# Kernel tuning notes

Hardware: AMD Instinct MI355X
Metric: run time of the kernel (lower is better)

Reference implementation:

```python
import jax, jax.numpy as jnp
import numpy as np

B = 128        # graphs
NPG = 64       # nodes per graph (num_node)
N = B * NPG    # total nodes = 8192
IN = 16        # in_channels
D = 128        # d_model
OUT = 64       # out_channels
CAT = IN * NPG + NPG * NPG  # 5120
EPS = 1e-5


def _lin_init(k, fi, fo):
    s = 1.0 / np.sqrt(fi)
    kw, kb = jax.random.split(k)
    W = jax.random.uniform(kw, (fi, fo), jnp.float32, -s, s)
    b = jax.random.uniform(kb, (fo,), jnp.float32, -s, s)
    return W, b


def setup_inputs() -> dict:
    key = jax.random.key(0)
    ks = jax.random.split(key, 10)
    x = jax.random.normal(ks[0], (N, IN), jnp.float32)
    # complete graph (all i->j pairs, incl. self loops) per graph, offset per graph
    ii = np.repeat(np.arange(NPG), NPG)
    jj = np.tile(np.arange(NPG), NPG)
    off = (np.arange(B) * NPG)[:, None]
    row = (ii[None, :] + off).reshape(-1)
    col = (jj[None, :] + off).reshape(-1)
    edge_index = jnp.asarray(np.stack([row, col]), jnp.int32)  # [2, E]
    E = edge_index.shape[1]
    edge_weight = jax.random.uniform(ks[1], (E,), jnp.float32)
    batch = jnp.repeat(jnp.arange(B, dtype=jnp.int32), NPG)
    W1, b1 = _lin_init(ks[2], IN, D)
    W2, b2 = _lin_init(ks[3], D, D)
    Wm0, bm0 = _lin_init(ks[4], D + CAT, D)
    Wm1, bm1 = _lin_init(ks[5], D, D)
    Wm2, bm2 = _lin_init(ks[6], D, D)
    Wout, bout = _lin_init(ks[7], D, OUT)
    ones = jnp.ones((D,), jnp.float32)
    zeros = jnp.zeros((D,), jnp.float32)
    return dict(x=x, edge_index=edge_index, edge_weight=edge_weight, batch=batch,
                W1=W1, b1=b1, W2=W2, b2=b2,
                Wm0=Wm0, bm0=bm0, g0=ones, be0=zeros,
                Wm1=Wm1, bm1=bm1, g1=ones, be1=zeros,
                Wm2=Wm2, bm2=bm2, g2=ones, be2=zeros,
                Wout=Wout, bout=bout)


def _gcn_conv(h_in, row, col, ew, W, b):
    # PyG GCNConv: linear first, then D^-1/2 (A) D^-1/2 aggregation (self loops already present)
    h = h_in @ W                                             # [N, F]
    deg = jax.ops.segment_sum(ew, col, num_segments=N)       # in-degree by edge weight
    dinv = jnp.where(deg > 0, jax.lax.rsqrt(deg), 0.0)
    norm = dinv[row] * ew * dinv[col]                        # [E]
    out = jax.ops.segment_sum(norm[:, None] * h[row], col, num_segments=N)
    return out + b


def _bn(h, g, b):
    # BatchNorm1d, training-mode math (biased variance), eps=1e-5
    m = jnp.mean(h, axis=0)
    v = jnp.var(h, axis=0)
    return g * (h - m) * jax.lax.rsqrt(v + EPS) + b


def reference(x, edge_index, edge_weight, batch,
              W1, b1, W2, b2,
              Wm0, bm0, g0, be0,
              Wm1, bm1, g1, be1,
              Wm2, bm2, g2, be2,
              Wout, bout):
    row, col = edge_index[0], edge_index[1]
    h = _gcn_conv(x, row, col, edge_weight, W1, b1)
    h = jax.nn.relu(h)
    h = _gcn_conv(h, row, col, edge_weight, W2, b2)
    # global_mean_pool
    sums = jax.ops.segment_sum(h, batch, num_segments=B)
    cnt = jax.ops.segment_sum(jnp.ones((N,), h.dtype), batch, num_segments=B)
    pooled = sums / cnt[:, None]
    pooled = jax.nn.relu(pooled)
    feat = jnp.concatenate([pooled, x.reshape(B, -1), edge_weight.reshape(B, -1)], axis=1)
    feat = jax.nn.relu(feat)
    h = _bn(jax.nn.relu(feat @ Wm0 + bm0), g0, be0)
    h = _bn(jax.nn.relu(h @ Wm1 + bm1), g1, be1)
    h = _bn(jax.nn.relu(h @ Wm2 + bm2), g2, be2)
    return h @ Wout + bout
```

## Files before the change

### kernel.cpp

```cpp
#include <hip/hip_runtime.h>

#define NG 128
#define NPG 64
#define IN 16
#define DM 128
#define NOUT 64
#define EPG 4096
#define NGEMM 160
#define BN_EPS 1e-5f

__global__ __launch_bounds__(256) void k_front(
    const float* __restrict__ x, const float* __restrict__ ew,
    const float* __restrict__ W1, const float* __restrict__ b1,
    const float* __restrict__ Wm0,
    float* __restrict__ z, float* __restrict__ part, float* __restrict__ stats)
{
    __shared__ __align__(16) float u[12544];
    const int b = blockIdx.x, t = threadIdx.x;

    if (b < 256) {
        float* ew_s   = u;
        float* x_s    = u + 4096;
        float* W1h_s  = u + 5120;
        float* P_s    = u + 6144;
        float* b1h_s  = u + 10240;
        float* dinv_s = u + 10304;
        float* t_s    = u + 10368;
        const int g = b >> 1, half = b & 1, fh0 = half * 64;
        if (b == 0) {
            for (int i = t; i < 768; i += 256) stats[i] = 0.f;
        }
        {
            const float4* ew4 = (const float4*)(ew + g * EPG);
            float4* ews4 = (float4*)ew_s;
            #pragma unroll
            for (int i = 0; i < 4; i++) ews4[t + 256 * i] = ew4[t + 256 * i];
            ((float4*)x_s)[t] = ((const float4*)(x + g * NPG * IN))[t];
        }
        for (int i = t; i < IN * 64; i += 256)
            W1h_s[i] = W1[(i >> 6) * DM + fh0 + (i & 63)];
        if (t < 64) b1h_s[t] = b1[fh0 + t];
        __syncthreads();

        if (t < NPG) {
            float s = 0.f;
            #pragma unroll 8
            for (int i = 0; i < NPG; i++) s += ew_s[i * NPG + t];
            dinv_s[t] = (s > 0.f) ? rsqrtf(s) : 0.f;
        }
        __syncthreads();

        {
            const int j = t & 63, q = t >> 6;
            const float dj = dinv_s[j];
            for (int i = q * 16; i < q * 16 + 16; i++) {
                float vv = ew_s[i * NPG + j] * dj;
                #pragma unroll
                for (int off = 32; off > 0; off >>= 1) vv += __shfl_down(vv, off, 64);
                if (j == 0) t_s[i] = dinv_s[i] * vv * (1.f / 64.f);
            }
        }

        {
            const int f = t & 63, ih = t >> 6;
            for (int i = ih * 16; i < ih * 16 + 16; i++) {
                float acc = 0.f;
                #pragma unroll
                for (int k = 0; k < IN; k++) acc += x_s[i * IN + k] * W1h_s[k * 64 + f];
                P_s[i * 64 + f] = acc;
            }
        }
        __syncthreads();

        for (int i = t; i < EPG; i += 256) ew_s[i] *= dinv_s[i >> 6];
        __syncthreads();

        {
            const int j = t & 63, q = t >> 6, fb = q * 16;
            float acc[16];
            #pragma unroll
            for (int uu = 0; uu < 16; uu++) acc[uu] = 0.f;
            for (int i = 0; i < NPG; i++) {
                const float w = ew_s[i * NPG + j];
                const float4* p4 = (const float4*)(P_s + i * 64 + fb);
                #pragma unroll
                for (int u4 = 0; u4 < 4; u4++) {
                    float4 p = p4[u4];
                    acc[4 * u4 + 0] += w * p.x;
                    acc[4 * u4 + 1] += w * p.y;
                    acc[4 * u4 + 2] += w * p.z;
                    acc[4 * u4 + 3] += w * p.w;
                }
            }
            const float dj = dinv_s[j], tj = t_s[j];
            #pragma unroll
            for (int uu = 0; uu < 16; uu++) {
                float h = fmaxf(dj * acc[uu] + b1h_s[fb + uu], 0.f);
                float zv = tj * h;
                #pragma unroll
                for (int off = 32; off > 0; off >>= 1) zv += __shfl_down(zv, off, 64);
                if (j == 0) z[g * DM + fh0 + fb + uu] = zv;
            }
        }
    } else {
        const int c = b - 256;
        const int kc = c >> 1, fh = c & 1;
        float* a_s = u;
        float* b_s = u + 8448;

        const float* src; int stride, off;
        if (kc < 16) { src = x;  stride = 1024; off = kc * 64; }
        else         { src = ew; stride = 4096; off = (kc - 16) * 64; }
        const int K0 = 128 + kc * 64;

        #pragma unroll 4
        for (int it = 0; it < 32; it++) {
            int idx = it * 256 + t;
            int gg = idx >> 6, k = idx & 63;
            a_s[k * 132 + gg] = fmaxf(src[gg * stride + off + k], 0.f);
        }
        #pragma unroll 4
        for (int it = 0; it < 16; it++) {
            int idx = it * 256 + t;
            int k = idx >> 6, fl = idx & 63;
            b_s[k * 64 + fl] = Wm0[(K0 + k) * 128 + fh * 64 + fl];
        }
        __syncthreads();

        const int gthr = t & 31, fthr = t >> 5;
        const int g0 = gthr * 4, f0 = fthr * 8;
        float acc[4][8];
        #pragma unroll
        for (int i = 0; i < 4; i++)
            #pragma unroll
            for (int jx = 0; jx < 8; jx++) acc[i][jx] = 0.f;

        #pragma unroll 4
        for (int k = 0; k < 64; k++) {
            const float4 a4  = *(const float4*)(a_s + k * 132 + g0);
            const float4 c0v = *(const float4*)(b_s + k * 64 + f0);
            const float4 c1v = *(const float4*)(b_s + k * 64 + f0 + 4);
            const float av[4] = {a4.x, a4.y, a4.z, a4.w};
            const float bv[8] = {c0v.x, c0v.y, c0v.z, c0v.w, c1v.x, c1v.y, c1v.z, c1v.w};
            #pragma unroll
            for (int i = 0; i < 4; i++)
                #pragma unroll
                for (int jx = 0; jx < 8; jx++) acc[i][jx] += av[i] * bv[jx];
        }

        float* pp = part + c * 8192;
        #pragma unroll
        for (int i = 0; i < 4; i++) {
            float4* o = (float4*)(pp + (g0 + i) * 64 + f0);
            o[0] = make_float4(acc[i][0], acc[i][1], acc[i][2], acc[i][3]);
            o[1] = make_float4(acc[i][4], acc[i][5], acc[i][6], acc[i][7]);
        }
    }
}

__global__ __launch_bounds__(256) void k_reduce_bn0(
    const float* __restrict__ part, const float* __restrict__ zbuf,
    const float* __restrict__ W2, const float* __restrict__ b2,
    const float* __restrict__ Wm0, const float* __restrict__ bm0,
    float* __restrict__ v0, float* __restrict__ stats0)
{
    __shared__ __align__(16) float W2_s[16384];
    __shared__ __align__(16) float z_s[512];
    __shared__ float Wm0s[2048];
    __shared__ float pooled_s[4 * 130];
    __shared__ float pps[64];
    __shared__ float r1[256];
    __shared__ float sv[64], sv2[64];

    const int bx = blockIdx.x, t = threadIdx.x;
    const int fgrp = bx & 7, gt = bx >> 3;
    const int fsub = t & 15, gl = (t >> 4) & 3, ch = t >> 6;
    const int f = fgrp * 16 + fsub, g = gt * 4 + gl;
    const int fh = f >> 6, fl = f & 63;

    const float* p = part + (size_t)(2 * (ch * 20) + fh) * 8192 + g * 64 + fl;
    float v = 0.f;
    #pragma unroll 5
    for (int cc = 0; cc < 20; cc++) v += p[(size_t)cc * 2 * 8192];

    {
        const float4* w24 = (const float4*)W2;
        float4* w2s4 = (float4*)W2_s;
        #pragma unroll
        for (int i = 0; i < 16; i++) w2s4[t + 256 * i] = w24[t + 256 * i];
        if (t < 128) ((float4*)z_s)[t] = ((const float4*)(zbuf + gt * 512))[t];
        for (int idx = t; idx < 2048; idx += 256) {
            int k = idx >> 4, fs = idx & 15;
            Wm0s[idx] = Wm0[k * DM + fgrp * 16 + fs];
        }
    }
    r1[t] = v;
    __syncthreads();

    {
        const int gp = t >> 6, k0 = t & 63;
        float a0 = 0.f, a1 = 0.f;
        #pragma unroll 4
        for (int m = 0; m < DM; m++) {
            const float zm = z_s[gp * DM + m];
            a0 += zm * W2_s[m * DM + k0];
            a1 += zm * W2_s[m * DM + k0 + 64];
        }
        pooled_s[gp * 130 + k0]      = fmaxf(a0 + b2[k0], 0.f);
        pooled_s[gp * 130 + k0 + 64] = fmaxf(a1 + b2[k0 + 64], 0.f);
    }
    __syncthreads();

    if (t < 64) {
        const int gl2 = t >> 4, fs = t & 15;
        float a = 0.f;
        #pragma unroll 8
        for (int k = 0; k < DM; k++) a += pooled_s[gl2 * 130 + k] * Wm0s[k * 16 + fs];
        pps[t] = a;
    }
    __syncthreads();

    if (ch == 0) {
        v = r1[t] + r1[t + 64] + r1[t + 128] + r1[t + 192]
          + bm0[f] + pps[t];
        v = fmaxf(v, 0.f);
        v0[g * DM + f] = v;
        sv[t] = v; sv2[t] = v * v;
    }
    __syncthreads();
    if (t < 16) {
        float s1 = sv[t] + sv[t + 16] + sv[t + 32] + sv[t + 48];
        float s2 = sv2[t] + sv2[t + 16] + sv2[t + 32] + sv2[t + 48];
        atomicAdd(&stats0[(fgrp * 16 + t) * 2], s1);
        atomicAdd(&stats0[(fgrp * 16 + t) * 2 + 1], s2);
    }
}

__global__ __launch_bounds__(256) void k_mlp(
    const float* __restrict__ vin, const float* __restrict__ statsin,
    const float* __restrict__ gbn, const float* __restrict__ bbn,
    const float* __restrict__ W, const float* __restrict__ bias,
    float* __restrict__ vout, float* __restrict__ statsout)
{
    __shared__ float h_s[128 * 129];
    __shared__ float wcol[128];
    __shared__ float scale_s[128], shift_s[128];
    __shared__ float pc[128];
    __shared__ float rr[4];
    const int f = blockIdx.x, t = threadIdx.x;
    if (t < 128) {
        float s1 = statsin[t * 2], s2 = statsin[t * 2 + 1];
        float m = s1 * (1.f / 128.f);
        float var = s2 * (1.f / 128.f) - m * m;
        float sc = gbn[t] * rsqrtf(var + BN_EPS);
        scale_s[t] = sc;
        shift_s[t] = bbn[t] - m * sc;
        wcol[t] = W[t * 128 + f];
    }
    __syncthreads();
    #pragma unroll 4
    for (int it = 0; it < 16; it++) {
        int idx = it * 256 + t;
        int g = idx >> 5, k4 = (idx & 31) * 4;
        float4 vv = ((const float4*)vin)[idx];
        float* hp = h_s + g * 129 + k4;
        hp[0] = vv.x * scale_s[k4 + 0] + shift_s[k4 + 0];
        hp[1] = vv.y * scale_s[k4 + 1] + shift_s[k4 + 1];
        hp[2] = vv.z * scale_s[k4 + 2] + shift_s[k4 + 2];
        hp[3] = vv.w * scale_s[k4 + 3] + shift_s[k4 + 3];
    }
    __syncthreads();
    const int g = t & 127, kh = t >> 7;
    float acc = 0.f;
    #pragma unroll 8
    for (int k = kh * 64; k < kh * 64 + 64; k++) acc += h_s[g * 129 + k] * wcol[k];
    if (kh) pc[g] = acc;
    __syncthreads();
    if (t < 128) {
        float v = fmaxf(acc + pc[t] + bias[f], 0.f);
        vout[t * 128 + f] = v;
        float s1 = v, s2 = v * v;
        #pragma unroll
        for (int off = 32; off > 0; off >>= 1) {
            s1 += __shfl_down(s1, off, 64);
            s2 += __shfl_down(s2, off, 64);
        }
        if ((t & 63) == 0) { rr[(t >> 6) * 2] = s1; rr[(t >> 6) * 2 + 1] = s2; }
    }
    __syncthreads();
    if (t == 0) {
        statsout[f * 2]     = rr[0] + rr[2];
        statsout[f * 2 + 1] = rr[1] + rr[3];
    }
}

__global__ __launch_bounds__(128) void k_out(
    const float* __restrict__ vin, const float* __restrict__ statsin,
    const float* __restrict__ gbn, const float* __restrict__ bbn,
    const float* __restrict__ Wo, const float* __restrict__ bo,
    float* __restrict__ out)
{
    __shared__ __align__(16) float Wo_s[128 * 64];
    __shared__ float vrow[2][128];
    __shared__ float scale_s[128], shift_s[128];
    const int b = blockIdx.x, t = threadIdx.x, g0 = b * 2;
    {
        float s1 = statsin[t * 2], s2 = statsin[t * 2 + 1];
        float m = s1 * (1.f / 128.f);
        float var = s2 * (1.f / 128.f) - m * m;
        float sc = gbn[t] * rsqrtf(var + BN_EPS);
        scale_s[t] = sc;
        shift_s[t] = bbn[t] - m * sc;
    }
    __syncthreads();
    {
        const float4* wo4 = (const float4*)Wo;
        float4* wos4 = (float4*)Wo_s;
        #pragma unroll
        for (int it = 0; it < 16; it++) wos4[it * 128 + t] = wo4[it * 128 + t];
    }
    if (t < 64) {
        int g2 = t >> 5, k4 = (t & 31) * 4;
        float4 vv = ((const float4*)(vin + g0 * 128))[t];
        vrow[g2][k4 + 0] = vv.x * scale_s[k4 + 0] + shift_s[k4 + 0];
        vrow[g2][k4 + 1] = vv.y * scale_s[k4 + 1] + shift_s[k4 + 1];
        vrow[g2][k4 + 2] = vv.z * scale_s[k4 + 2] + shift_s[k4 + 2];
        vrow[g2][k4 + 3] = vv.w * scale_s[k4 + 3] + shift_s[k4 + 3];
    }
    __syncthreads();
    const int g2 = t >> 6, o = t & 63;
    float acc = bo[o];
    #pragma unroll 8
    for (int k = 0; k < 128; k++) acc += vrow[g2][k] * Wo_s[k * 64 + o];
    out[(g0 + g2) * NOUT + o] = acc;
}

extern "C" void kernel_launch(void* const* d_in, const int* in_sizes, int n_in,
                              void* d_out, int out_size, void* d_ws, size_t ws_size,
                              hipStream_t stream)
{
    const float* x   = (const float*)d_in[0];
    const float* ew  = (const float*)d_in[2];
    const float* W1  = (const float*)d_in[4];
    const float* b1  = (const float*)d_in[5];
    const float* W2  = (const float*)d_in[6];
    const float* b2  = (const float*)d_in[7];
    const float* Wm0 = (const float*)d_in[8];
    const float* bm0 = (const float*)d_in[9];
    const float* g0  = (const float*)d_in[10];
    const float* be0 = (const float*)d_in[11];
    const float* Wm1 = (const float*)d_in[12];
    const float* bm1 = (const float*)d_in[13];
    const float* g1  = (const float*)d_in[14];
    const float* be1 = (const float*)d_in[15];
    const float* Wm2 = (const float*)d_in[16];
    const float* bm2 = (const float*)d_in[17];
    const float* g2  = (const float*)d_in[18];
    const float* be2 = (const float*)d_in[19];
    const float* Wo  = (const float*)d_in[20];
    const float* bo  = (const float*)d_in[21];

    float* ws     = (float*)d_ws;
    float* zbuf   = ws;
    float* part   = zbuf + 16384;
    float* v0     = part + NGEMM * 8192;
    float* v1     = v0 + 16384;
    float* v2     = v1 + 16384;
    float* stats  = v2 + 16384;

    k_front<<<256 + NGEMM, 256, 0, stream>>>(x, ew, W1, b1, Wm0, zbuf, part, stats);
    k_reduce_bn0<<<256, 256, 0, stream>>>(part, zbuf, W2, b2, Wm0, bm0, v0, stats);
    k_mlp<<<128, 256, 0, stream>>>(v0, stats,       g0, be0, Wm1, bm1, v1, stats + 256);
    k_mlp<<<128, 256, 0, stream>>>(v1, stats + 256, g1, be1, Wm2, bm2, v2, stats + 512);
    k_out<<<NOUT, 128, 0, stream>>>(v2, stats + 512, g2, be2, Wo, bo, (float*)d_out);
}
```

Baseline: 140.4 us.

## Fuse all stages into one persistent kernel with grid-wide atomic barriers

Replaces five kernel launches with a single 256-block kernel that runs the GCN front, the split-K Wm0 GEMM, the BN0 reduction, two MLP stages and the output layer in sequence, separated by software grid barriers built on atomics. The Wm0 GEMM is re-split into 256 chunks of 40 K-values so every block does both the front work and a GEMM slice. The MLP stages now split graphs across two blocks per feature and accumulate BN statistics with atomics. A memset zeroes the stats and barrier counters beforehand. This removes launch gaps and kernel boundaries, at the cost of relying on all 256 blocks being co-resident and of serialising the front and GEMM work inside each block.

```diff
diff --git a/kernel.cpp b/kernel.cpp
--- a/kernel.cpp
+++ b/kernel.cpp
@@ -6,19 +6,104 @@
 #define DM 128
 #define NOUT 64
 #define EPG 4096
-#define NGEMM 160
 #define BN_EPS 1e-5f
-
-__global__ __launch_bounds__(256) void k_front(
+#define NBLK 256
+
+__device__ __forceinline__ void gbar(unsigned* bar, int idx) {
+    __syncthreads();
+    if (threadIdx.x == 0) {
+        __threadfence();
+        __hip_atomic_fetch_add(&bar[idx], 1u, __ATOMIC_ACQ_REL, __HIP_MEMORY_SCOPE_AGENT);
+        while (__hip_atomic_load(&bar[idx], __ATOMIC_ACQUIRE, __HIP_MEMORY_SCOPE_AGENT) < (unsigned)NBLK) {
+            __builtin_amdgcn_s_sleep(2);
+        }
+        __threadfence();
+    }
+    __syncthreads();
+}
+
+__device__ __forceinline__ void mlp_stage(
+    float* u, const float* __restrict__ vin, const float* __restrict__ statsin,
+    const float* __restrict__ gbn, const float* __restrict__ bbn,
+    const float* __restrict__ W, const float* __restrict__ bias,
+    float* __restrict__ vout, float* __restrict__ statsout)
+{
+    float* scale_s = u;
+    float* shift_s = u + 128;
+    float* wcol    = u + 256;
+    float* pc      = u + 384;
+    float* h_s     = u + 640;
+    const int b = blockIdx.x, t = threadIdx.x;
+    const int f = b & 127, gh = b >> 7;
+    if (t < 128) {
+        float s1 = statsin[t * 2], s2 = statsin[t * 2 + 1];
+        float m = s1 * (1.f / 128.f);
+        float var = s2 * (1.f / 128.f) - m * m;
+        float sc = gbn[t] * rsqrtf(var + BN_EPS);
+        scale_s[t] = sc;
+        shift_s[t] = bbn[t] - m * sc;
+        wcol[t] = W[t * 128 + f];
+    }
+    __syncthreads();
+    const int g0r = gh * 64;
+    const float4* vin4 = (const float4*)(vin + g0r * 128);
+    #pragma unroll
+    for (int it = 0; it < 8; ++it) {
+        int idx = it * 256 + t;
+        int gl = idx >> 5, k4 = (idx & 31) * 4;
+        float4 vv = vin4[idx];
+        float* hp = h_s + gl * 129 + k4;
+        hp[0] = vv.x * scale_s[k4 + 0] + shift_s[k4 + 0];
+        hp[1] = vv.y * scale_s[k4 + 1] + shift_s[k4 + 1];
+        hp[2] = vv.z * scale_s[k4 + 2] + shift_s[k4 + 2];
+        hp[3] = vv.w * scale_s[k4 + 3] + shift_s[k4 + 3];
+    }
+    __syncthreads();
+    {
+        const int gl = t & 63, kh = t >> 6;
+        float acc = 0.f;
+        #pragma unroll 8
+        for (int k = kh * 32; k < kh * 32 + 32; ++k) acc += h_s[gl * 129 + k] * wcol[k];
+        pc[gl * 4 + kh] = acc;
+    }
+    __syncthreads();
+    if (t < 64) {
+        float v = fmaxf(pc[t * 4] + pc[t * 4 + 1] + pc[t * 4 + 2] + pc[t * 4 + 3]
+                        + bias[f], 0.f);
+        vout[(size_t)(g0r + t) * 128 + f] = v;
+        float s1 = v, s2 = v * v;
+        #pragma unroll
+        for (int off = 32; off > 0; off >>= 1) {
+            s1 += __shfl_down(s1, off, 64);
+            s2 += __shfl_down(s2, off, 64);
+        }
+        if (t == 0) {
+            atomicAdd(&statsout[f * 2], s1);
+            atomicAdd(&statsout[f * 2 + 1], s2);
+        }
+    }
+}
+
+__global__ __launch_bounds__(256, 2) void k_all(
     const float* __restrict__ x, const float* __restrict__ ew,
     const float* __restrict__ W1, const float* __restrict__ b1,
-    const float* __restrict__ Wm0,
-    float* __restrict__ z, float* __restrict__ part, float* __restrict__ stats)
+    const float* __restrict__ W2, const float* __restrict__ b2,
+    const float* __restrict__ Wm0, const float* __restrict__ bm0,
+    const float* __restrict__ g0bn, const float* __restrict__ be0,
+    const float* __restrict__ Wm1, const float* __restrict__ bm1,
+    const float* __restrict__ g1bn, const float* __restrict__ be1,
+    const float* __restrict__ Wm2, const float* __restrict__ bm2,
+    const float* __restrict__ g2bn, const float* __restrict__ be2,
+    const float* __restrict__ Wo, const float* __restrict__ bo,
+    float* __restrict__ z, float* __restrict__ part,
+    float* __restrict__ v0, float* __restrict__ v1, float* __restrict__ v2,
+    float* __restrict__ stats, unsigned* __restrict__ bar,
+    float* __restrict__ out)
 {
-    __shared__ __align__(16) float u[12544];
+    __shared__ __align__(16) float u[19968];
     const int b = blockIdx.x, t = threadIdx.x;
 
-    if (b < 256) {
+    {
         float* ew_s   = u;
         float* x_s    = u + 4096;
         float* W1h_s  = u + 5120;
@@ -27,9 +112,6 @@
         float* dinv_s = u + 10304;
         float* t_s    = u + 10368;
         const int g = b >> 1, half = b & 1, fh0 = half * 64;
-        if (b == 0) {
-            for (int i = t; i < 768; i += 256) stats[i] = 0.f;
-        }
         {
             const float4* ew4 = (const float4*)(ew + g * EPG);
             float4* ews4 = (float4*)ew_s;
@@ -60,7 +142,6 @@
                 if (j == 0) t_s[i] = dinv_s[i] * vv * (1.f / 64.f);
             }
         }
-
         {
             const int f = t & 63, ih = t >> 6;
             for (int i = ih * 16; i < ih * 16 + 16; i++) {
@@ -102,28 +183,27 @@
                 if (j == 0) z[g * DM + fh0 + fb + uu] = zv;
             }
         }
-    } else {
-        const int c = b - 256;
-        const int kc = c >> 1, fh = c & 1;
+        __syncthreads();
+    }
+
+    {
+        const int kc = b >> 1, fh = b & 1;
+        const int K0 = kc * 40;
         float* a_s = u;
-        float* b_s = u + 8448;
-
-        const float* src; int stride, off;
-        if (kc < 16) { src = x;  stride = 1024; off = kc * 64; }
-        else         { src = ew; stride = 4096; off = (kc - 16) * 64; }
-        const int K0 = 128 + kc * 64;
+        float* b_s = u + 5280;
 
         #pragma unroll 4
-        for (int it = 0; it < 32; it++) {
+        for (int it = 0; it < 20; ++it) {
             int idx = it * 256 + t;
-            int gg = idx >> 6, k = idx & 63;
-            a_s[k * 132 + gg] = fmaxf(src[gg * stride + off + k], 0.f);
+            int k = idx >> 7, gg = idx & 127;
+            int K = K0 + k;
+            float val = (K < 1024) ? x[gg * 1024 + K] : ew[gg * 4096 + (K - 1024)];
+            a_s[k * 132 + gg] = fmaxf(val, 0.f);
         }
         #pragma unroll 4
-        for (int it = 0; it < 16; it++) {
-            int idx = it * 256 + t;
+        for (int idx = t; idx < 2560; idx += 256) {
             int k = idx >> 6, fl = idx & 63;
-            b_s[k * 64 + fl] = Wm0[(K0 + k) * 128 + fh * 64 + fl];
+            b_s[k * 64 + fl] = Wm0[(128 + K0 + k) * 128 + fh * 64 + fl];
         }
         __syncthreads();
 
@@ -136,7 +216,7 @@
             for (int jx = 0; jx < 8; jx++) acc[i][jx] = 0.f;
 
         #pragma unroll 4
-        for (int k = 0; k < 64; k++) {
+        for (int k = 0; k < 40; k++) {
             const float4 a4  = *(const float4*)(a_s + k * 132 + g0);
             const float4 c0v = *(const float4*)(b_s + k * 64 + f0);
             const float4 c1v = *(const float4*)(b_s + k * 64 + f0 + 4);
@@ -147,8 +227,7 @@
                 #pragma unroll
                 for (int jx = 0; jx < 8; jx++) acc[i][jx] += av[i] * bv[jx];
         }
-
-        float* pp = part + c * 8192;
+        float* pp = part + (size_t)b * 8192;
         #pragma unroll
         for (int i = 0; i < 4; i++) {
             float4* o = (float4*)(pp + (g0 + i) * 64 + f0);
@@ -156,183 +235,121 @@
             o[1] = make_float4(acc[i][4], acc[i][5], acc[i][6], acc[i][7]);
         }
     }
-}
-
-__global__ __launch_bounds__(256) void k_reduce_bn0(
-    const float* __restrict__ part, const float* __restrict__ zbuf,
-    const float* __restrict__ W2, const float* __restrict__ b2,
-    const float* __restrict__ Wm0, const float* __restrict__ bm0,
-    float* __restrict__ v0, float* __restrict__ stats0)
-{
-    __shared__ __align__(16) float W2_s[16384];
-    __shared__ __align__(16) float z_s[512];
-    __shared__ float Wm0s[2048];
-    __shared__ float pooled_s[4 * 130];
-    __shared__ float pps[64];
-    __shared__ float r1[256];
-    __shared__ float sv[64], sv2[64];
-
-    const int bx = blockIdx.x, t = threadIdx.x;
-    const int fgrp = bx & 7, gt = bx >> 3;
-    const int fsub = t & 15, gl = (t >> 4) & 3, ch = t >> 6;
-    const int f = fgrp * 16 + fsub, g = gt * 4 + gl;
-    const int fh = f >> 6, fl = f & 63;
-
-    const float* p = part + (size_t)(2 * (ch * 20) + fh) * 8192 + g * 64 + fl;
-    float v = 0.f;
-    #pragma unroll 5
-    for (int cc = 0; cc < 20; cc++) v += p[(size_t)cc * 2 * 8192];
+    gbar(bar, 0);
 
     {
-        const float4* w24 = (const float4*)W2;
-        float4* w2s4 = (float4*)W2_s;
-        #pragma unroll
-        for (int i = 0; i < 16; i++) w2s4[t + 256 * i] = w24[t + 256 * i];
-        if (t < 128) ((float4*)z_s)[t] = ((const float4*)(zbuf + gt * 512))[t];
-        for (int idx = t; idx < 2048; idx += 256) {
-            int k = idx >> 4, fs = idx & 15;
-            Wm0s[idx] = Wm0[k * DM + fgrp * 16 + fs];
-        }
-    }
-    r1[t] = v;
-    __syncthreads();
-
-    {
-        const int gp = t >> 6, k0 = t & 63;
-        float a0 = 0.f, a1 = 0.f;
-        #pragma unroll 4
-        for (int m = 0; m < DM; m++) {
-            const float zm = z_s[gp * DM + m];
-            a0 += zm * W2_s[m * DM + k0];
-            a1 += zm * W2_s[m * DM + k0 + 64];
-        }
-        pooled_s[gp * 130 + k0]      = fmaxf(a0 + b2[k0], 0.f);
-        pooled_s[gp * 130 + k0 + 64] = fmaxf(a1 + b2[k0 + 64], 0.f);
-    }
-    __syncthreads();
-
-    if (t < 64) {
-        const int gl2 = t >> 4, fs = t & 15;
-        float a = 0.f;
+        float* W2_s     = u;
+        float* z_s      = u + 16384;
+        float* Wm0s     = u + 16896;
+        float* pooled_s = u + 18944;
+        float* pps      = u + 19464;
+        float* r1       = u + 19528;
+        float* sv       = u + 19784;
+        float* sv2      = u + 19848;
+        const int fgrp = b & 7, gt = b >> 3;
+        const int fsub = t & 15, gl = (t >> 4) & 3, ch = t >> 6;
+        const int f = fgrp * 16 + fsub, g = gt * 4 + gl;
+        const int fh = f >> 6, fl = f & 63;
+
+        const float* p = part + (size_t)(2 * (ch * 32) + fh) * 8192 + g * 64 + fl;
+        float v = 0.f;
         #pragma unroll 8
-        for (int k = 0; k < DM; k++) a += pooled_s[gl2 * 130 + k] * Wm0s[k * 16 + fs];
-        pps[t] = a;
-    }
-    __syncthreads();
-
-    if (ch == 0) {
-        v = r1[t] + r1[t + 64] + r1[t + 128] + r1[t + 192]
-          + bm0[f] + pps[t];
-        v = fmaxf(v, 0.f);
-        v0[g * DM + f] = v;
-        sv[t] = v; sv2[t] = v * v;
-    }
-    __syncthreads();
-    if (t < 16) {
-        float s1 = sv[t] + sv[t + 16] + sv[t + 32] + sv[t + 48];
-        float s2 = sv2[t] + sv2[t + 16] + sv2[t + 32] + sv2[t + 48];
-        atomicAdd(&stats0[(fgrp * 16 + t) * 2], s1);
-        atomicAdd(&stats0[(fgrp * 16 + t) * 2 + 1], s2);
-    }
-}
-
-__global__ __launch_bounds__(256) void k_mlp(
-    const float* __restrict__ vin, const float* __restrict__ statsin,
-    const float* __restrict__ gbn, const float* __restrict__ bbn,
-    const float* __restrict__ W, const float* __restrict__ bias,
-    float* __restrict__ vout, float* __restrict__ statsout)
-{
-    __shared__ float h_s[128 * 129];
-    __shared__ float wcol[128];
-    __shared__ float scale_s[128], shift_s[128];
-    __shared__ float pc[128];
-    __shared__ float rr[4];
-    const int f = blockIdx.x, t = threadIdx.x;
-    if (t < 128) {
-        float s1 = statsin[t * 2], s2 = statsin[t * 2 + 1];
-        float m = s1 * (1.f / 128.f);
-        float var = s2 * (1.f / 128.f) - m * m;
-        float sc = gbn[t] * rsqrtf(var + BN_EPS);
-        scale_s[t] = sc;
-        shift_s[t] = bbn[t] - m * sc;
-        wcol[t] = W[t * 128 + f];
-    }
-    __syncthreads();
-    #pragma unroll 4
-    for (int it = 0; it < 16; it++) {
-        int idx = it * 256 + t;
-        int g = idx >> 5, k4 = (idx & 31) * 4;
-        float4 vv = ((const float4*)vin)[idx];
-        float* hp = h_s + g * 129 + k4;
-        hp[0] = vv.x * scale_s[k4 + 0] + shift_s[k4 + 0];
-        hp[1] = vv.y * scale_s[k4 + 1] + shift_s[k4 + 1];
-        hp[2] = vv.z * scale_s[k4 + 2] + shift_s[k4 + 2];
-        hp[3] = vv.w * scale_s[k4 + 3] + shift_s[k4 + 3];
-    }
-    __syncthreads();
-    const int g = t & 127, kh = t >> 7;
-    float acc = 0.f;
-    #pragma unroll 8
-    for (int k = kh * 64; k < kh * 64 + 64; k++) acc += h_s[g * 129 + k] * wcol[k];
-    if (kh) pc[g] = acc;
-    __syncthreads();
-    if (t < 128) {
-        float v = fmaxf(acc + pc[t] + bias[f], 0.f);
-        vout[t * 128 + f] = v;
-        float s1 = v, s2 = v * v;
-        #pragma unroll
-        for (int off = 32; off > 0; off >>= 1) {
-            s1 += __shfl_down(s1, off, 64);
-            s2 += __shfl_down(s2, off, 64);
-        }
-        if ((t & 63) == 0) { rr[(t >> 6) * 2] = s1; rr[(t >> 6) * 2 + 1] = s2; }
-    }
-    __syncthreads();
-    if (t == 0) {
-        statsout[f * 2]     = rr[0] + rr[2];
-        statsout[f * 2 + 1] = rr[1] + rr[3];
-    }
-}
-
-__global__ __launch_bounds__(128) void k_out(
-    const float* __restrict__ vin, const float* __restrict__ statsin,
-    const float* __restrict__ gbn, const float* __restrict__ bbn,
-    const float* __restrict__ Wo, const float* __restrict__ bo,
-    float* __restrict__ out)
-{
-    __shared__ __align__(16) float Wo_s[128 * 64];
-    __shared__ float vrow[2][128];
-    __shared__ float scale_s[128], shift_s[128];
-    const int b = blockIdx.x, t = threadIdx.x, g0 = b * 2;
-    {
-        float s1 = statsin[t * 2], s2 = statsin[t * 2 + 1];
-        float m = s1 * (1.f / 128.f);
-        float var = s2 * (1.f / 128.f) - m * m;
-        float sc = gbn[t] * rsqrtf(var + BN_EPS);
-        scale_s[t] = sc;
-        shift_s[t] = bbn[t] - m * sc;
-    }
-    __syncthreads();
-    {
-        const float4* wo4 = (const float4*)Wo;
-        float4* wos4 = (float4*)Wo_s;
-        #pragma unroll
-        for (int it = 0; it < 16; it++) wos4[it * 128 + t] = wo4[it * 128 + t];
-    }
-    if (t < 64) {
-        int g2 = t >> 5, k4 = (t & 31) * 4;
-        float4 vv = ((const float4*)(vin + g0 * 128))[t];
-        vrow[g2][k4 + 0] = vv.x * scale_s[k4 + 0] + shift_s[k4 + 0];
-        vrow[g2][k4 + 1] = vv.y * scale_s[k4 + 1] + shift_s[k4 + 1];
-        vrow[g2][k4 + 2] = vv.z * scale_s[k4 + 2] + shift_s[k4 + 2];
-        vrow[g2][k4 + 3] = vv.w * scale_s[k4 + 3] + shift_s[k4 + 3];
-    }
-    __syncthreads();
-    const int g2 = t >> 6, o = t & 63;
-    float acc = bo[o];
-    #pragma unroll 8
-    for (int k = 0; k < 128; k++) acc += vrow[g2][k] * Wo_s[k * 64 + o];
-    out[(g0 + g2) * NOUT + o] = acc;
+        for (int cc = 0; cc < 32; cc++) v += p[(size_t)cc * 16384];
+
+        {
+            const float4* w24 = (const float4*)W2;
+            float4* w2s4 = (float4*)W2_s;
+            #pragma unroll
+            for (int i = 0; i < 16; i++) w2s4[t + 256 * i] = w24[t + 256 * i];
+            if (t < 128) ((float4*)z_s)[t] = ((const float4*)(z + gt * 512))[t];
+            for (int idx = t; idx < 2048; idx += 256) {
+                int k = idx >> 4, fs = idx & 15;
+                Wm0s[idx] = Wm0[k * DM + fgrp * 16 + fs];
+            }
+        }
+        r1[t] = v;
+        __syncthreads();
+
+        {
+            const int gp = t >> 6, k0 = t & 63;
+            float a0 = 0.f, a1 = 0.f;
+            #pragma unroll 4
+            for (int m = 0; m < DM; m++) {
+                const float zm = z_s[gp * DM + m];
+                a0 += zm * W2_s[m * DM + k0];
+                a1 += zm * W2_s[m * DM + k0 + 64];
+            }
+            pooled_s[gp * 130 + k0]      = fmaxf(a0 + b2[k0], 0.f);
+            pooled_s[gp * 130 + k0 + 64] = fmaxf(a1 + b2[k0 + 64], 0.f);
+        }
+        __syncthreads();
+        if (t < 64) {
+            const int gl2 = t >> 4, fs = t & 15;
+            float a = 0.f;
+            #pragma unroll 8
+            for (int k = 0; k < DM; k++) a += pooled_s[gl2 * 130 + k] * Wm0s[k * 16 + fs];
+            pps[t] = a;
+        }
+        __syncthreads();
+        if (ch == 0) {
+            v = r1[t] + r1[t + 64] + r1[t + 128] + r1[t + 192] + bm0[f] + pps[t];
+            v = fmaxf(v, 0.f);
+            v0[g * DM + f] = v;
+            sv[t] = v; sv2[t] = v * v;
+        }
+        __syncthreads();
+        if (t < 16) {
+            float s1 = sv[t] + sv[t + 16] + sv[t + 32] + sv[t + 48];
+            float s2 = sv2[t] + sv2[t + 16] + sv2[t + 32] + sv2[t + 48];
+            atomicAdd(&stats[(fgrp * 16 + t) * 2], s1);
+            atomicAdd(&stats[(fgrp * 16 + t) * 2 + 1], s2);
+        }
+    }
+    gbar(bar, 1);
+
+    mlp_stage(u, v0, stats,       g0bn, be0, Wm1, bm1, v1, stats + 256);
+    gbar(bar, 2);
+    mlp_stage(u, v1, stats + 256, g1bn, be1, Wm2, bm2, v2, stats + 512);
+    gbar(bar, 3);
+
+    if (b < 128) {
+        float* scale_s = u;
+        float* shift_s = u + 128;
+        float* Wo_s    = u + 256;
+        float* vrow    = u + 8448;
+        const int g = b;
+        const float* statsin = stats + 512;
+        if (t < 128) {
+            float s1 = statsin[t * 2], s2 = statsin[t * 2 + 1];
+            float m = s1 * (1.f / 128.f);
+            float var = s2 * (1.f / 128.f) - m * m;
+            float sc = g2bn[t] * rsqrtf(var + BN_EPS);
+            scale_s[t] = sc;
+            shift_s[t] = be2[t] - m * sc;
+        }
+        __syncthreads();
+        {
+            const float4* wo4 = (const float4*)Wo;
+            float4* wos4 = (float4*)Wo_s;
+            #pragma unroll
+            for (int it = 0; it < 8; it++) wos4[it * 256 + t] = wo4[it * 256 + t];
+        }
+        if (t < 32) {
+            float4 vv = ((const float4*)(v2 + g * 128))[t];
+            int k4 = t * 4;
+            vrow[k4 + 0] = vv.x * scale_s[k4 + 0] + shift_s[k4 + 0];
+            vrow[k4 + 1] = vv.y * scale_s[k4 + 1] + shift_s[k4 + 1];
+            vrow[k4 + 2] = vv.z * scale_s[k4 + 2] + shift_s[k4 + 2];
+            vrow[k4 + 3] = vv.w * scale_s[k4 + 3] + shift_s[k4 + 3];
+        }
+        __syncthreads();
+        if (t < 64) {
+            float acc = bo[t];
+            #pragma unroll 8
+            for (int k = 0; k < 128; k++) acc += vrow[k] * Wo_s[k * 64 + t];
+            out[g * NOUT + t] = acc;
+        }
+    }
 }
 
 extern "C" void kernel_launch(void* const* d_in, const int* in_sizes, int n_in,
@@ -360,17 +377,19 @@
     const float* Wo  = (const float*)d_in[20];
     const float* bo  = (const float*)d_in[21];
 
-    float* ws     = (float*)d_ws;
-    float* zbuf   = ws;
-    float* part   = zbuf + 16384;
-    float* v0     = part + NGEMM * 8192;
-    float* v1     = v0 + 16384;
-    float* v2     = v1 + 16384;
-    float* stats  = v2 + 16384;
-
-    k_front<<<256 + NGEMM, 256, 0, stream>>>(x, ew, W1, b1, Wm0, zbuf, part, stats);
-    k_reduce_bn0<<<256, 256, 0, stream>>>(part, zbuf, W2, b2, Wm0, bm0, v0, stats);
-    k_mlp<<<128, 256, 0, stream>>>(v0, stats,       g0, be0, Wm1, bm1, v1, stats + 256);
-    k_mlp<<<128, 256, 0, stream>>>(v1, stats + 256, g1, be1, Wm2, bm2, v2, stats + 512);
-    k_out<<<NOUT, 128, 0, stream>>>(v2, stats + 512, g2, be2, Wo, bo, (float*)d_out);
+    float* ws    = (float*)d_ws;
+    float* zbuf  = ws;
+    float* part  = zbuf + 16384;
+    float* v0    = part + 256 * 8192;
+    float* v1    = v0 + 16384;
+    float* v2    = v1 + 16384;
+    float* stats = v2 + 16384;
+    unsigned* bar = (unsigned*)(stats + 768);
+
+    hipMemsetAsync(stats, 0, (768 + 8) * sizeof(float), stream);
+
+    k_all<<<NBLK, 256, 0, stream>>>(
+        x, ew, W1, b1, W2, b2, Wm0, bm0, g0, be0,
+        Wm1, bm1, g1, be1, Wm2, bm2, g2, be2, Wo, bo,
+        zbuf, part, v0, v1, v2, stats, bar, (float*)d_out);
 }
```

Result: slower. 235.3 us (+67.6%).

## Process whole graph per block with register-tiled GCN matmuls in k_front

Applied to the files above, without the earlier changes.

Each GCN block in k_front now handles a full graph with all 128 features instead of splitting the features across two blocks, which halves the GCN block count and removes the duplicated edge-weight load and degree computation. The x@W1 and aggregation products are rewritten as 4x8 register-tiled outer products using float4 shared-memory loads. The per-feature wavefront shuffle reduction for z is replaced by a shared-memory partial-sum reduction. Shared memory use grows, which may reduce occupancy, and there are fewer blocks to spread across the GPU.

```diff
diff --git a/kernel.cpp b/kernel.cpp
--- a/kernel.cpp
+++ b/kernel.cpp
@@ -15,18 +15,19 @@
     const float* __restrict__ Wm0,
     float* __restrict__ z, float* __restrict__ part, float* __restrict__ stats)
 {
-    __shared__ __align__(16) float u[12544];
+    __shared__ __align__(16) float u[15616];
     const int b = blockIdx.x, t = threadIdx.x;
 
-    if (b < 256) {
+    if (b < 128) {
         float* ew_s   = u;
         float* x_s    = u + 4096;
-        float* W1h_s  = u + 5120;
-        float* P_s    = u + 6144;
-        float* b1h_s  = u + 10240;
-        float* dinv_s = u + 10304;
-        float* t_s    = u + 10368;
-        const int g = b >> 1, half = b & 1, fh0 = half * 64;
+        float* W1_s   = u + 5120;
+        float* P_s    = u + 7168;
+        float* b1_s   = u + 15360;
+        float* dinv_s = u + 15488;
+        float* t_s    = u + 15552;
+        float* zp     = u + 4096;
+        const int g = b;
         if (b == 0) {
             for (int i = t; i < 768; i += 256) stats[i] = 0.f;
         }
@@ -35,11 +36,16 @@
             float4* ews4 = (float4*)ew_s;
             #pragma unroll
             for (int i = 0; i < 4; i++) ews4[t + 256 * i] = ew4[t + 256 * i];
-            ((float4*)x_s)[t] = ((const float4*)(x + g * NPG * IN))[t];
-        }
-        for (int i = t; i < IN * 64; i += 256)
-            W1h_s[i] = W1[(i >> 6) * DM + fh0 + (i & 63)];
-        if (t < 64) b1h_s[t] = b1[fh0 + t];
+            const int xi = t & 63, k4 = (t >> 6) * 4;
+            float4 xv = *(const float4*)(x + g * NPG * IN + xi * IN + k4);
+            x_s[(k4 + 0) * 64 + xi] = xv.x;
+            x_s[(k4 + 1) * 64 + xi] = xv.y;
+            x_s[(k4 + 2) * 64 + xi] = xv.z;
+            x_s[(k4 + 3) * 64 + xi] = xv.w;
+            ((float4*)W1_s)[t]       = ((const float4*)W1)[t];
+            ((float4*)W1_s)[t + 256] = ((const float4*)W1)[t + 256];
+            if (t < 128) b1_s[t] = b1[t];
+        }
         __syncthreads();
 
         if (t < NPG) {
@@ -60,15 +66,34 @@
                 if (j == 0) t_s[i] = dinv_s[i] * vv * (1.f / 64.f);
             }
         }
+        __syncthreads();
 
         {
-            const int f = t & 63, ih = t >> 6;
-            for (int i = ih * 16; i < ih * 16 + 16; i++) {
-                float acc = 0.f;
-                #pragma unroll
-                for (int k = 0; k < IN; k++) acc += x_s[i * IN + k] * W1h_s[k * 64 + f];
-                P_s[i * 64 + f] = acc;
+            const int it = t & 15, ft = t >> 4;
+            const int i0 = it * 4, f0 = ft * 8;
+            float accp[4][8];
+            #pragma unroll
+            for (int a = 0; a < 4; a++)
+                #pragma unroll
+                for (int c = 0; c < 8; c++) accp[a][c] = 0.f;
+            #pragma unroll
+            for (int k = 0; k < IN; k++) {
+                const float4 a4  = *(const float4*)(x_s + k * 64 + i0);
+                const float4 b0v = *(const float4*)(W1_s + k * DM + f0);
+                const float4 b1v = *(const float4*)(W1_s + k * DM + f0 + 4);
+                const float av[4] = {a4.x, a4.y, a4.z, a4.w};
+                const float bv[8] = {b0v.x, b0v.y, b0v.z, b0v.w, b1v.x, b1v.y, b1v.z, b1v.w};
+                #pragma unroll
+                for (int a = 0; a < 4; a++)
+                    #pragma unroll
+                    for (int c = 0; c < 8; c++) accp[a][c] += av[a] * bv[c];
             }
+            #pragma unroll
+            for (int a = 0; a < 4; a++) {
+                float4* o = (float4*)(P_s + (i0 + a) * DM + f0);
+                o[0] = make_float4(accp[a][0], accp[a][1], accp[a][2], accp[a][3]);
+                o[1] = make_float4(accp[a][4], accp[a][5], accp[a][6], accp[a][7]);
+            }
         }
         __syncthreads();
 
@@ -76,34 +101,51 @@
         __syncthreads();
 
         {
-            const int j = t & 63, q = t >> 6, fb = q * 16;
-            float acc[16];
-            #pragma unroll
-            for (int uu = 0; uu < 16; uu++) acc[uu] = 0.f;
-            for (int i = 0; i < NPG; i++) {
-                const float w = ew_s[i * NPG + j];
-                const float4* p4 = (const float4*)(P_s + i * 64 + fb);
-                #pragma unroll
-                for (int u4 = 0; u4 < 4; u4++) {
-                    float4 p = p4[u4];
-                    acc[4 * u4 + 0] += w * p.x;
-                    acc[4 * u4 + 1] += w * p.y;
-                    acc[4 * u4 + 2] += w * p.z;
-                    acc[4 * u4 + 3] += w * p.w;
+            const int jt = t & 15, ft = t >> 4;
+            const int j0 = jt * 4, f0 = ft * 8;
+            float acc[4][8];
+            #pragma unroll
+            for (int a = 0; a < 4; a++)
+                #pragma unroll
+                for (int c = 0; c < 8; c++) acc[a][c] = 0.f;
+            #pragma unroll 4
+            for (int k = 0; k < 64; k++) {
+                const float4 a4  = *(const float4*)(ew_s + k * 64 + j0);
+                const float4 b0v = *(const float4*)(P_s + k * DM + f0);
+                const float4 b1v = *(const float4*)(P_s + k * DM + f0 + 4);
+                const float av[4] = {a4.x, a4.y, a4.z, a4.w};
+                const float bv[8] = {b0v.x, b0v.y, b0v.z, b0v.w, b1v.x, b1v.y, b1v.z, b1v.w};
+                #pragma unroll
+                for (int a = 0; a < 4; a++)
+                    #pragma unroll
+                    for (int c = 0; c < 8; c++) acc[a][c] += av[a] * bv[c];
+            }
+            float zpart[8];
+            #pragma unroll
+            for (int c = 0; c < 8; c++) zpart[c] = 0.f;
+            #pragma unroll
+            for (int a = 0; a < 4; a++) {
+                const float dj = dinv_s[j0 + a], tj = t_s[j0 + a];
+                #pragma unroll
+                for (int c = 0; c < 8; c++) {
+                    float h = fmaxf(dj * acc[a][c] + b1_s[f0 + c], 0.f);
+                    zpart[c] += tj * h;
                 }
             }
-            const float dj = dinv_s[j], tj = t_s[j];
-            #pragma unroll
-            for (int uu = 0; uu < 16; uu++) {
-                float h = fmaxf(dj * acc[uu] + b1h_s[fb + uu], 0.f);
-                float zv = tj * h;
-                #pragma unroll
-                for (int off = 32; off > 0; off >>= 1) zv += __shfl_down(zv, off, 64);
-                if (j == 0) z[g * DM + fh0 + fb + uu] = zv;
-            }
+            float4* zo = (float4*)(zp + jt * 132 + f0);
+            zo[0] = make_float4(zpart[0], zpart[1], zpart[2], zpart[3]);
+            zo[1] = make_float4(zpart[4], zpart[5], zpart[6], zpart[7]);
+        }
+        __syncthreads();
+
+        if (t < 128) {
+            float s = 0.f;
+            #pragma unroll
+            for (int jt = 0; jt < 16; jt++) s += zp[jt * 132 + t];
+            z[g * DM + t] = s;
         }
     } else {
-        const int c = b - 256;
+        const int c = b - 128;
         const int kc = c >> 1, fh = c & 1;
         float* a_s = u;
         float* b_s = u + 8448;
@@ -210,7 +252,6 @@
         pooled_s[gp * 130 + k0 + 64] = fmaxf(a1 + b2[k0 + 64], 0.f);
     }
     __syncthreads();
-
     if (t < 64) {
         const int gl2 = t >> 4, fs = t & 15;
         float a = 0.f;
@@ -219,10 +260,8 @@
         pps[t] = a;
     }
     __syncthreads();
-
     if (ch == 0) {
-        v = r1[t] + r1[t + 64] + r1[t + 128] + r1[t + 192]
-          + bm0[f] + pps[t];
+        v = r1[t] + r1[t + 64] + r1[t + 128] + r1[t + 192] + bm0[f] + pps[t];
         v = fmaxf(v, 0.f);
         v0[g * DM + f] = v;
         sv[t] = v; sv2[t] = v * v;
@@ -368,7 +407,7 @@
     float* v2     = v1 + 16384;
     float* stats  = v2 + 16384;
 
-    k_front<<<256 + NGEMM, 256, 0, stream>>>(x, ew, W1, b1, Wm0, zbuf, part, stats);
+    k_front<<<128 + NGEMM, 256, 0, stream>>>(x, ew, W1, b1, Wm0, zbuf, part, stats);
     k_reduce_bn0<<<256, 256, 0, stream>>>(part, zbuf, W2, b2, Wm0, bm0, v0, stats);
     k_mlp<<<128, 256, 0, stream>>>(v0, stats,       g0, be0, Wm1, bm1, v1, stats + 256);
     k_mlp<<<128, 256, 0, stream>>>(v1, stats + 256, g1, be1, Wm2, bm2, v2, stats + 512);
```

New measurement: 136.9 us. -2.5%, faster.
